# Performance work log

Hardware: AMD Instinct MI355X
Metric: run time of the kernel (lower is better)

The kernel has to match this reference:

```python
import jax, jax.numpy as jnp
import numpy as np

D_MODEL = 512
N_HEADS = 8
HIDDEN = 2048  # mlp_ratio * d_model
B, N = 2, 1024

# 2^dim sign-flip frames for FrameAveraging(dim=2)
_FRAME_OPS = jnp.array([[1., 1.], [1., -1.], [-1., 1.], [-1., -1.]], jnp.float32)


def _ln(x, g, b, eps=1e-5):
    mu = jnp.mean(x, axis=-1, keepdims=True)
    var = jnp.mean((x - mu) ** 2, axis=-1, keepdims=True)
    return (x - mu) * jax.lax.rsqrt(var + eps) * g + b


def setup_inputs() -> dict:
    key = jax.random.key(0)
    ks = jax.random.split(key, 8)
    s = 0.02
    return {
        "token_embs": jax.random.normal(ks[0], (B, N, D_MODEL), jnp.float32),
        "coords": jax.random.normal(ks[1], (B, N, 2), jnp.float32),
        "padding_mask": jnp.zeros((B, N, N), jnp.bool_),
        "ln1_g": jnp.ones((D_MODEL,), jnp.float32),
        "ln1_b": jnp.zeros((D_MODEL,), jnp.float32),
        "w_qkv": jax.random.normal(ks[2], (D_MODEL, 3 * D_MODEL), jnp.float32) * s,
        "b_qkv": jnp.zeros((3 * D_MODEL,), jnp.float32),
        "w_edge": jax.random.normal(ks[3], (3, N_HEADS), jnp.float32) * s,
        "w_out": jax.random.normal(ks[4], (D_MODEL, D_MODEL), jnp.float32) * s,
        "b_out": jnp.zeros((D_MODEL,), jnp.float32),
        "ln2_g": jnp.ones((D_MODEL,), jnp.float32),
        "ln2_b": jnp.zeros((D_MODEL,), jnp.float32),
        "w1": jax.random.normal(ks[5], (D_MODEL, HIDDEN), jnp.float32) * s,
        "b1": jnp.zeros((HIDDEN,), jnp.float32),
        "w2": jax.random.normal(ks[6], (HIDDEN, D_MODEL), jnp.float32) * s,
        "b2": jnp.zeros((D_MODEL,), jnp.float32),
    }


def _block(x, coords, pad_mask, ln1_g, ln1_b, w_qkv, b_qkv, w_edge, w_out, b_out,
           ln2_g, ln2_b, w1, b1, w2, b2):
    Bb, Nn, C = x.shape
    H = w_edge.shape[1]
    d = C // H
    scale = d ** -0.5
    nf = _FRAME_OPS.shape[0]

    # ---- attention QKV ----
    qkv = _ln(x, ln1_g, ln1_b) @ w_qkv + b_qkv
    q, k, v = jnp.split(qkv, 3, axis=-1)
    q = q.reshape(Bb, Nn, H, d).transpose(0, 2, 1, 3) * scale  # (B,H,N,d)
    k = k.reshape(Bb, Nn, H, d).transpose(0, 2, 1, 3)
    v = v.reshape(Bb, Nn, H, d).transpose(0, 2, 1, 3)
    attn = jnp.einsum('bhnd,bhmd->bhnm', q, k)

    # ---- pairwise radial coords + frame averaging ----
    rc = coords[:, :, None, :] - coords[:, None, :, :]           # (B,N,N,2)
    rnorm = jnp.linalg.norm(rc, axis=-1).reshape(Bb * Nn, Nn, 1)
    rc = rc.reshape(Bb * Nn, Nn, 2)                              # (M,N,2)
    valid = (~pad_mask).reshape(Bb * Nn, Nn)
    m = valid.astype(rc.dtype)[..., None]                        # (M,N,1)
    center = jnp.sum(rc * m, axis=1) / jnp.sum(m, axis=1)        # masked mean
    Xc = (rc - center[:, None]) * m                              # (M,N,2)
    Cov = jnp.einsum('mni,mnj->mij', Xc, Xc)                     # (M,2,2)
    _, V = jnp.linalg.eigh(jax.lax.stop_gradient(Cov))           # PCA frame (detached)
    F_ops = _FRAME_OPS[None, :, None, :] * V[:, None]            # (M,nf,2,2) sign-flipped eigvecs
    h = jnp.einsum('moji,mpj->mopi', F_ops, Xc) * m[:, None]     # (M,nf,N,2)

    feat = jnp.concatenate(
        [h, jnp.broadcast_to(rnorm[:, None], (Bb * Nn, nf, Nn, 1))], axis=-1)  # (M,nf,N,3)
    bias = jnp.einsum('monk,kh->monh', feat, w_edge).mean(axis=1)  # (M,N,H)
    bias = bias.reshape(Bb, Nn, Nn, H).transpose(0, 3, 1, 2)       # (B,H,N,N)

    attn = attn + bias
    attn = jnp.where(pad_mask[:, None], jnp.float32(-1e9), attn)
    attn = jax.nn.softmax(attn, axis=-1)
    o = jnp.einsum('bhnm,bhmd->bhnd', attn, v)
    o = o.transpose(0, 2, 1, 3).reshape(Bb, Nn, C) @ w_out + b_out

    x = x + o
    y = _ln(x, ln2_g, ln2_b)
    y = jax.nn.gelu(y @ w1 + b1, approximate=False) @ w2 + b2
    return x + y


def reference(token_embs, coords, padding_mask, ln1_g, ln1_b, w_qkv, b_qkv, w_edge,
              w_out, b_out, ln2_g, ln2_b, w1, b1, w2, b2):
    return _block(token_embs, coords, padding_mask, ln1_g, ln1_b, w_qkv, b_qkv,
                  w_edge, w_out, b_out, ln2_g, ln2_b, w1, b1, w2, b2)
```

## Files before the change

kernel.cpp:

```cpp
#include <hip/hip_runtime.h>
#include <hip/hip_bf16.h>
#include <math.h>

#define NHEADS 8
#define NTOK   1024
#define MTOK   2048

typedef __attribute__((ext_vector_type(8))) short  sh8;
typedef __attribute__((ext_vector_type(8))) __bf16 bf16x8;
typedef __attribute__((ext_vector_type(4))) float  f32x4;
typedef __attribute__((ext_vector_type(4))) unsigned int u32x4;

__device__ __forceinline__ short f2bf(float v) {
    return __builtin_bit_cast(short, __float2bfloat16(v));
}
__device__ __forceinline__ float bf2f(short v) {
    return __builtin_bit_cast(float, ((unsigned)(unsigned short)v) << 16);
}
__device__ __forceinline__ float ex2(float v) {
    return __builtin_amdgcn_exp2f(v);
}
__device__ __forceinline__ f32x4 mfma16(sh8 a, sh8 b, f32x4 c) {
    return __builtin_amdgcn_mfma_f32_16x16x32_bf16(
        __builtin_bit_cast(bf16x8, a), __builtin_bit_cast(bf16x8, b), c, 0, 0, 0);
}
__device__ __forceinline__ void aload16(void* lds, const void* g) {
    __builtin_amdgcn_global_load_lds(
        (const __attribute__((address_space(1))) unsigned int*)g,
        (__attribute__((address_space(3))) unsigned int*)lds, 16, 0, 0);
}

#define LOG2E 1.4426950408889634f

template<bool FUSE>
__global__ __launch_bounds__(256) void ln_bf16(const float* __restrict__ x,
    const float* __restrict__ g, const float* __restrict__ bta, short* __restrict__ y,
    const float* __restrict__ bias2, float* __restrict__ resout)
{
    int row = blockIdx.x, t = threadIdx.x;
    const float* xr = x + (size_t)row * 512;
    float2 v = *reinterpret_cast<const float2*>(&xr[t*2]);
    float s = v.x + v.y, ss = v.x*v.x + v.y*v.y;
    #pragma unroll
    for (int m = 1; m < 64; m <<= 1) { s += __shfl_xor(s, m); ss += __shfl_xor(ss, m); }
    __shared__ float red[8];
    int wid = t >> 6, lane = t & 63;
    if (!lane) { red[wid] = s; red[4+wid] = ss; }
    __syncthreads();
    s = red[0]+red[1]+red[2]+red[3]; ss = red[4]+red[5]+red[6]+red[7];
    float mu = s*(1.f/512), var = ss*(1.f/512) - mu*mu, rs = rsqrtf(var + 1e-5f);
    float2 gg = *reinterpret_cast<const float2*>(&g[t*2]);
    float2 bb = *reinterpret_cast<const float2*>(&bta[t*2]);
    short2 o; o.x = f2bf((v.x-mu)*rs*gg.x + bb.x); o.y = f2bf((v.y-mu)*rs*gg.y + bb.y);
    *reinterpret_cast<short2*>(&y[(size_t)row*512 + t*2]) = o;
    if (FUSE) {
        float2 b2 = *reinterpret_cast<const float2*>(&bias2[t*2]);
        float2 ro = {v.x + b2.x, v.y + b2.y};
        *reinterpret_cast<float2*>(&resout[(size_t)row*512 + t*2]) = ro;
    }
}

__global__ __launch_bounds__(256) void wconv2x(
    const float* __restrict__ W0, short* __restrict__ WT0, int K0, int N0, int nb0,
    const float* __restrict__ W1, short* __restrict__ WT1, int K1, int N1)
{
    const float* W; short* WT; int K, N, bid;
    if ((int)blockIdx.x < nb0) { W = W0; WT = WT0; K = K0; N = N0; bid = blockIdx.x; }
    else                       { W = W1; WT = WT1; K = K1; N = N1; bid = blockIdx.x - nb0; }
    int nbx = N >> 5;
    int bn = (bid % nbx) * 32, bk = (bid / nbx) * 32;
    __shared__ float t[32][33];
    int c = threadIdx.x & 31, r8 = threadIdx.x >> 5;
    #pragma unroll
    for (int i = 0; i < 4; ++i) {
        int r = r8 + i*8;
        t[r][c] = W[(size_t)(bk + r)*N + bn + c];
    }
    __syncthreads();
    #pragma unroll
    for (int i = 0; i < 4; ++i) {
        int r = r8 + i*8;
        WT[(size_t)(bn + r)*K + bk + c] = f2bf(t[c][r]);
    }
}

__global__ __launch_bounds__(256) void prep(const float* __restrict__ coords,
    const unsigned char* __restrict__ mask, short* __restrict__ rnP,
    unsigned long long* __restrict__ mbP)
{
    __shared__ float2 kc_s[64];
    __shared__ float2 qc_s[16];
    int bid = blockIdx.x;
    int bqt = bid >> 4, jt = bid & 15;
    int b = bqt >> 6, qt = bqt & 63;
    int t = threadIdx.x, w = t >> 6, lane = t & 63;
    int lr = lane & 15, lg = lane >> 4;

    if (t < 64)            kc_s[t]      = *reinterpret_cast<const float2*>(&coords[(size_t)(b*1024 + jt*64 + t)*2]);
    else if (t < 80)       qc_s[t - 64] = *reinterpret_cast<const float2*>(&coords[(size_t)(b*1024 + qt*16 + (t - 64))*2]);
    __syncthreads();

    float2 qc = qc_s[lr];
    short4 o;
    short* op = &o.x;
    #pragma unroll
    for (int r = 0; r < 4; ++r) {
        float2 kc = kc_s[w*16 + lg*4 + r];
        float dx = qc.x - kc.x, dy = qc.y - kc.y;
        op[r] = f2bf(sqrtf(dx*dx + dy*dy));
    }
    *reinterpret_cast<short4*>(&rnP[(size_t)((bid*4 + w)*256) + lane*4]) = o;

    #pragma unroll
    for (int i = 0; i < 4; ++i) {
        int q = w*4 + i;
        unsigned char v = mask[(size_t)(b*1024 + qt*16 + q)*NTOK + jt*64 + lane];
        unsigned long long bits = __ballot(v != 0);
        if (!lane) mbP[(size_t)bid*16 + q] = bits;
    }
}

template<int EPI, bool OUTBF, bool BIAS_ROW, int SPLITK, bool QSC, int NT>
__global__ __launch_bounds__(256) void gemm64(
    const short* __restrict__ A, const short* __restrict__ BT,
    const float* __restrict__ bias, const float* __restrict__ res,
    void* __restrict__ Cout, int M, int N, int K, int nbx)
{
    __shared__ sh8 As8[3][512];
    __shared__ sh8 Bs8[3][512];
    int tid = threadIdx.x;
    int w = tid >> 6, lane = tid & 63, lr = lane & 15, lg = lane >> 4;
    int wr = w >> 1, wc = w & 1;
    int cpx = gridDim.x >> 3;
    int swz = (blockIdx.x & 7)*cpx + (blockIdx.x >> 3);
    int bx = swz % nbx, by = swz / nbx;
    int bm0 = by*64, bn0 = bx*64;
    int kbeg = (K / SPLITK) * blockIdx.z;

    f32x4 zero = {0.f,0.f,0.f,0.f};
    f32x4 acc[2][2];
    #pragma unroll
    for (int m = 0; m < 2; ++m)
        #pragma unroll
        for (int n = 0; n < 2; ++n) acc[m][n] = zero;

    #define STAGE(buf, k0) { \
        _Pragma("unroll") \
        for (int it = 0; it < 2; ++it) { \
            int s = tid + it*256; \
            int r = s >> 3, g = s & 7; \
            int ksw = (k0) + ((g ^ (r & 7)) << 3); \
            aload16(&As8[buf][s], A  + (size_t)(bm0 + r)*K + ksw); \
            aload16(&Bs8[buf][s], BT + (size_t)(bn0 + r)*K + ksw); \
        } }

    STAGE(0, kbeg)
    if (NT > 1) STAGE(1, kbeg + 64)

    #pragma unroll
    for (int t = 0; t < NT; ++t) {
        if (t + 1 < NT) asm volatile("s_waitcnt vmcnt(4)" ::: "memory");
        else            asm volatile("s_waitcnt vmcnt(0)" ::: "memory");
        __builtin_amdgcn_s_barrier();
        __builtin_amdgcn_sched_barrier(0);
        int buf = t % 3;
        sh8 af[2][2], bfv[2][2];
        #pragma unroll
        for (int m = 0; m < 2; ++m) {
            int R = wr*32 + m*16 + lr;
            #pragma unroll
            for (int s = 0; s < 2; ++s) af[m][s] = As8[buf][R*8 + ((s*4+lg) ^ (R & 7))];
        }
        #pragma unroll
        for (int n = 0; n < 2; ++n) {
            int R = wc*32 + n*16 + lr;
            #pragma unroll
            for (int s = 0; s < 2; ++s) bfv[n][s] = Bs8[buf][R*8 + ((s*4+lg) ^ (R & 7))];
        }
        if (t + 2 < NT) STAGE((t+2)%3, kbeg + (t+2)*64)
        #pragma unroll
        for (int m = 0; m < 2; ++m)
            #pragma unroll
            for (int n = 0; n < 2; ++n)
                #pragma unroll
                for (int s = 0; s < 2; ++s)
                    acc[m][n] = mfma16(af[m][s], bfv[n][s], acc[m][n]);
        asm volatile("s_waitcnt lgkmcnt(0)" ::: "memory");
    }
    #undef STAGE

    #pragma unroll
    for (int m = 0; m < 2; ++m) {
        #pragma unroll
        for (int n = 0; n < 2; ++n) {
            #pragma unroll
            for (int r = 0; r < 4; ++r) {
                int row = bm0 + wr*32 + m*16 + lg*4 + r;
                int col = bn0 + wc*32 + n*16 + lr;
                if (EPI == 3) {
                    atomicAdd((float*)Cout + (size_t)row*N + col, acc[m][n][r]);
                } else {
                    float v = acc[m][n][r] + (BIAS_ROW ? bias[row] : bias[col]);
                    if (QSC && col < 512) v *= (0.125f * LOG2E);
                    if (EPI == 1) v += res[(size_t)row*N + col];
                    if (EPI == 2) v = 0.5f * v * (1.0f + erff(v * 0.70710678f));
                    if (OUTBF) ((short*)Cout)[(size_t)row*N + col] = f2bf(v);
                    else       ((float*)Cout)[(size_t)row*N + col] = v;
                }
            }
        }
    }
}

__global__ __launch_bounds__(256) void attn_reg(
    const short* __restrict__ qk, const short* __restrict__ vt,
    const short* __restrict__ rnP, const unsigned long long* __restrict__ mbP,
    const float* __restrict__ w_edge, short* __restrict__ OpA,
    short* __restrict__ OpB, float* __restrict__ ml)
{
    __shared__ sh8 Ks8[2][512];
    __shared__ sh8 Vs8[2][512];

    int cpx = gridDim.x >> 3;
    int swz = (blockIdx.x & 7)*cpx + (blockIdx.x >> 3);
    int w = threadIdx.x >> 6, lane = threadIdx.x & 63;
    int lr = lane & 15, lg = lane >> 4;
    int qb = swz & 15;
    int h  = (swz >> 4) & 7;
    int b  = (swz >> 7) & 1;
    int ks = swz >> 8;

    const int q0 = qb*64 + w*16;
    const int qrow0 = b*NTOK + q0;
    const int jt0 = ks*4;
    const int bqt = b*64 + qb*4 + w;

    sh8 qf[2];
    #pragma unroll
    for (int s = 0; s < 2; ++s)
        qf[s] = *reinterpret_cast<const sh8*>(qk + (size_t)(qrow0 + lr)*1024 + h*64 + s*32 + lg*8);

    float we2l = w_edge[2*NHEADS + h] * LOG2E;

    float m_i = -1e30f, l_lane = 0.f;
    f32x4 zero = {0.f,0.f,0.f,0.f};
    f32x4 accO[4];
    #pragma unroll
    for (int n = 0; n < 4; ++n) accO[n] = zero;

    const short* kbase = qk + 512 + h*64;
    const short* vbase = vt + (size_t)h*64*2048 + b*NTOK;
    int sr = threadIdx.x >> 3, sg = threadIdx.x & 7;
    int sx = (sg ^ (sr & 7)) << 3;

    #define ASTAGE(bf, jt) { \
        aload16(&Ks8[bf][threadIdx.x],       kbase + (size_t)(b*NTOK + (jt)*64 + sr)*1024 + sx); \
        aload16(&Ks8[bf][threadIdx.x + 256], kbase + (size_t)(b*NTOK + (jt)*64 + sr + 32)*1024 + sx); \
        aload16(&Vs8[bf][threadIdx.x],       vbase + (size_t)sr*2048 + (jt)*64 + sx); \
        aload16(&Vs8[bf][threadIdx.x + 256], vbase + (size_t)(sr + 32)*2048 + (jt)*64 + sx); \
    }

    short4 rn_reg[2][4];
    unsigned long long mr_reg[2];
    #define RMLOAD(bf, jt) { \
        _Pragma("unroll") \
        for (int n = 0; n < 4; ++n) \
            rn_reg[bf][n] = *reinterpret_cast<const short4*>( \
                &rnP[(size_t)(((bqt*16 + (jt))*4 + n)*256) + lane*4]); \
        mr_reg[bf] = mbP[(size_t)(bqt*16 + (jt))*16 + lr]; \
    }

    ASTAGE(0, jt0)
    RMLOAD(0, jt0)

    #pragma unroll
    for (int t = 0; t < 4; ++t) {
        if (t == 0) asm volatile("s_waitcnt vmcnt(0)" ::: "memory");
        else        asm volatile("s_waitcnt vmcnt(5)" ::: "memory");
        __builtin_amdgcn_s_barrier();
        __builtin_amdgcn_sched_barrier(0);
        int buf = t & 1;

        if (t + 1 < 4) {
            ASTAGE(buf ^ 1, jt0 + t + 1)
            RMLOAD(buf ^ 1, jt0 + t + 1)
        }

        f32x4 Sv[4];
        #pragma unroll
        for (int n = 0; n < 4; ++n) {
            int kcol = n*16 + lr;
            sh8 k0v = Ks8[buf][kcol*8 + (lg       ^ (kcol & 7))];
            sh8 k1v = Ks8[buf][kcol*8 + ((4 + lg) ^ (kcol & 7))];
            Sv[n] = mfma16(k1v, qf[1], mfma16(k0v, qf[0], zero));
        }

        #pragma unroll
        for (int n = 0; n < 4; ++n) {
            short4 rn4 = rn_reg[buf][n];
            Sv[n][0] = fmaf(bf2f(rn4.x), we2l, Sv[n][0]);
            Sv[n][1] = fmaf(bf2f(rn4.y), we2l, Sv[n][1]);
            Sv[n][2] = fmaf(bf2f(rn4.z), we2l, Sv[n][2]);
            Sv[n][3] = fmaf(bf2f(rn4.w), we2l, Sv[n][3]);
        }

        float mx = Sv[0][0];
        #pragma unroll
        for (int n = 0; n < 4; ++n)
            #pragma unroll
            for (int r = 0; r < 4; ++r) mx = fmaxf(mx, Sv[n][r]);
        mx = fmaxf(mx, __shfl_xor(mx, 16));
        mx = fmaxf(mx, __shfl_xor(mx, 32));
        float mnew = fmaxf(m_i, mx);
        float f = ex2(m_i - mnew);
        m_i = mnew;

        unsigned long long mr = mr_reg[buf];
        float ps = 0.f;
        unsigned pk[8];
        #pragma unroll
        for (int n = 0; n < 4; ++n) {
            float p_[4];
            #pragma unroll
            for (int r = 0; r < 4; ++r) {
                float p = ex2(Sv[n][r] - mnew);
                p = ((mr >> (n*16 + lg*4 + r)) & 1ull) ? 0.f : p;
                ps += p;
                p_[r] = p;
            }
            pk[2*n]   = ((unsigned)(unsigned short)f2bf(p_[1]) << 16) | (unsigned short)f2bf(p_[0]);
            pk[2*n+1] = ((unsigned)(unsigned short)f2bf(p_[3]) << 16) | (unsigned short)f2bf(p_[2]);
        }
        l_lane = l_lane * f + ps;

        int src0 = lr + ((lg & 1) << 5);
        int src1 = src0 + 16;
        sh8 pa[2];
        #pragma unroll
        for (int s = 0; s < 2; ++s) {
            int ns = 2*s + (lg >> 1);
            u32x4 dv;
            dv.x = (unsigned)__shfl((int)pk[2*ns],   src0);
            dv.y = (unsigned)__shfl((int)pk[2*ns+1], src0);
            dv.z = (unsigned)__shfl((int)pk[2*ns],   src1);
            dv.w = (unsigned)__shfl((int)pk[2*ns+1], src1);
            pa[s] = __builtin_bit_cast(sh8, dv);
        }

        float fb[4];
        #pragma unroll
        for (int r = 0; r < 4; ++r) fb[r] = __shfl(f, lg*4 + r);
        #pragma unroll
        for (int n = 0; n < 4; ++n)
            #pragma unroll
            for (int r = 0; r < 4; ++r) accO[n][r] *= fb[r];

        #pragma unroll
        for (int n = 0; n < 4; ++n) {
            int dcol = n*16 + lr;
            sh8 v0 = Vs8[buf][dcol*8 + (lg       ^ (dcol & 7))];
            sh8 v1 = Vs8[buf][dcol*8 + ((4 + lg) ^ (dcol & 7))];
            accO[n] = mfma16(pa[1], v1, mfma16(pa[0], v0, accO[n]));
        }

        asm volatile("s_waitcnt lgkmcnt(0)" ::: "memory");
    }
    #undef ASTAGE
    #undef RMLOAD

    l_lane += __shfl_xor(l_lane, 16);
    l_lane += __shfl_xor(l_lane, 32);

    short* Op = (ks < 2) ? OpA : OpB;
    #pragma unroll
    for (int r = 0; r < 4; ++r) {
        size_t row = (size_t)((ks & 1)*MTOK + qrow0 + lg*4 + r);
        #pragma unroll
        for (int n = 0; n < 4; ++n)
            Op[row*512 + h*64 + n*16 + lr] = f2bf(accO[n][r]);
    }
    if (lg == 0) {
        size_t mrow = (size_t)(ks*MTOK + qrow0 + lr);
        ml[(mrow*NHEADS + h)*2 + 0] = m_i;
        ml[(mrow*NHEADS + h)*2 + 1] = l_lane;
    }
}

__global__ __launch_bounds__(256) void attn_combine4(const short* __restrict__ OpA,
    const short* __restrict__ OpB, const float* __restrict__ ml,
    short* __restrict__ ob)
{
    int idx = blockIdx.x*256 + threadIdx.x;
    int tok = idx >> 7, dd = (idx & 127) * 4;
    int h = dd >> 6;
    float m[4], l[4];
    #pragma unroll
    for (int s = 0; s < 4; ++s) {
        m[s] = ml[(((size_t)s*MTOK + tok)*NHEADS + h)*2 + 0];
        l[s] = ml[(((size_t)s*MTOK + tok)*NHEADS + h)*2 + 1];
    }
    float mm = fmaxf(fmaxf(m[0], m[1]), fmaxf(m[2], m[3]));
    float wsum = 0.f, a0 = 0.f, a1 = 0.f, a2 = 0.f, a3 = 0.f;
    #pragma unroll
    for (int s = 0; s < 4; ++s) {
        float wv = ex2(m[s] - mm);
        wsum += wv * l[s];
        const short* Op = (s < 2) ? OpA : OpB;
        short4 p = *reinterpret_cast<const short4*>(&Op[((size_t)((s&1)*MTOK) + tok)*512 + dd]);
        a0 += bf2f(p.x)*wv; a1 += bf2f(p.y)*wv;
        a2 += bf2f(p.z)*wv; a3 += bf2f(p.w)*wv;
    }
    float inv = 1.f / wsum;
    short4 o;
    o.x = f2bf(a0*inv); o.y = f2bf(a1*inv);
    o.z = f2bf(a2*inv); o.w = f2bf(a3*inv);
    *reinterpret_cast<short4*>(&ob[(size_t)tok*512 + dd]) = o;
}

extern "C" void kernel_launch(void* const* d_in, const int* in_sizes, int n_in,
                              void* d_out, int out_size, void* d_ws, size_t ws_size,
                              hipStream_t stream)
{
    const float* x      = (const float*)d_in[0];
    const float* coords = (const float*)d_in[1];
    const unsigned char* mask = (const unsigned char*)d_in[2];
    const float* ln1_g = (const float*)d_in[3];
    const float* ln1_b = (const float*)d_in[4];
    const float* w_qkv = (const float*)d_in[5];
    const float* b_qkv = (const float*)d_in[6];
    const float* w_edge= (const float*)d_in[7];
    const float* w_out = (const float*)d_in[8];
    const float* b_out = (const float*)d_in[9];
    const float* ln2_g = (const float*)d_in[10];
    const float* ln2_b = (const float*)d_in[11];
    const float* w1    = (const float*)d_in[12];
    const float* b1    = (const float*)d_in[13];
    const float* w2    = (const float*)d_in[14];
    const float* b2    = (const float*)d_in[15];
    float* out = (float*)d_out;

    char* W = (char*)d_ws;
    const size_t MB = 1024*1024;
    float* x1    = (float*)(W);
    short* qk    = (short*)(W + 4*MB);
    short* vtb   = (short*)(W + 8*MB);
    short* woutT = (short*)(W + 10*MB);
    short* xln   = (short*)(W + 10*MB + 512*1024);
    short* wqkvT = (short*)(W + 12*MB + 512*1024);
    short* OpB   = (short*)(W + 10*MB + 512*1024);
    short* OpA   = (short*)(W + 14*MB + 512*1024);
    short* rnP   = (short*)(W + 18*MB + 512*1024);
    float* mlp   = (float*)(W + 22*MB + 512*1024);
    unsigned long long* mbP = (unsigned long long*)(W + 23*MB);
    short* ob    = (short*)(W + 6*MB);
    short* y     = xln;
    short* w1T   = (short*)(W + 4*MB);
    short* w2T   = (short*)(W + 8*MB);
    short* hid   = (short*)(W + 14*MB + 512*1024);

    prep<<<dim3(2048,1,1), 256, 0, stream>>>(coords, mask, rnP, mbP);
    wconv2x<<<dim3(1024,1,1), 256, 0, stream>>>(w_qkv, wqkvT, 512, 1536, 768,
                                                w_out, woutT, 512, 512);
    ln_bf16<false><<<MTOK, 256, 0, stream>>>(x, ln1_g, ln1_b, xln, nullptr, nullptr);
    gemm64<0,true,false,1,true,8><<<dim3(512,1,1), 256, 0, stream>>>(
        xln, wqkvT, b_qkv, nullptr, qk, MTOK, 1024, 512, 16);
    gemm64<0,true,true,1,false,8><<<dim3(256,1,1), 256, 0, stream>>>(
        wqkvT + (size_t)1024*512, xln, b_qkv + 1024, nullptr, vtb, 512, MTOK, 512, 32);
    attn_reg<<<dim3(1024,1,1), 256, 0, stream>>>(qk, vtb, rnP, mbP, w_edge, OpA, OpB, mlp);
    attn_combine4<<<dim3(1024,1,1), 256, 0, stream>>>(OpA, OpB, mlp, ob);
    gemm64<1,false,false,1,false,8><<<dim3(256,1,1), 256, 0, stream>>>(
        ob, woutT, b_out, x, x1, MTOK, 512, 512, 8);
    wconv2x<<<dim3(2048,1,1), 256, 0, stream>>>(w1, w1T, 512, 2048, 1024,
                                                w2, w2T, 2048, 512);
    ln_bf16<true><<<MTOK, 256, 0, stream>>>(x1, ln2_g, ln2_b, y, b2, out);
    gemm64<2,true,false,1,false,8><<<dim3(1024,1,1), 256, 0, stream>>>(
        y, w1T, b1, nullptr, hid, MTOK, 2048, 512, 32);
    gemm64<3,false,false,2,false,16><<<dim3(256,1,2), 256, 0, stream>>>(
        hid, w2T, nullptr, nullptr, out, MTOK, 512, 2048, 8);
}
```

Baseline: 92.84 us.

## Add 64x32 GEMM tiles, drop split-K atomics, lazy softmax rescale, packed bf16 cvt

Adds a gemm32n kernel with 64x32 output tiles and uses it for the V projection, the output projection and the second MLP GEMM. This doubles the block count on the narrow GEMMs and replaces the split-K atomicAdd path, whose residual and bias were pre-written by the fused LN, with a plain epilogue that adds bias and residual. In attention, the online-softmax rescale is skipped unless some row max grows by more than 8 (log2 domain), and probabilities are packed to bf16 with v_cvt_pk_bf16_f32. The lazy rescale lets p values reach up to 2^8, which risks bf16 precision loss, and the unsplit second MLP GEMM now runs a 32-step K loop per block.

Result: no change. 92.32 us (-0.6%).

```diff
diff --git a/kernel.cpp b/kernel.cpp
--- a/kernel.cpp
+++ b/kernel.cpp
@@ -32,10 +32,8 @@
 
 #define LOG2E 1.4426950408889634f
 
-template<bool FUSE>
 __global__ __launch_bounds__(256) void ln_bf16(const float* __restrict__ x,
-    const float* __restrict__ g, const float* __restrict__ bta, short* __restrict__ y,
-    const float* __restrict__ bias2, float* __restrict__ resout)
+    const float* __restrict__ g, const float* __restrict__ bta, short* __restrict__ y)
 {
     int row = blockIdx.x, t = threadIdx.x;
     const float* xr = x + (size_t)row * 512;
@@ -53,11 +51,6 @@
     float2 bb = *reinterpret_cast<const float2*>(&bta[t*2]);
     short2 o; o.x = f2bf((v.x-mu)*rs*gg.x + bb.x); o.y = f2bf((v.y-mu)*rs*gg.y + bb.y);
     *reinterpret_cast<short2*>(&y[(size_t)row*512 + t*2]) = o;
-    if (FUSE) {
-        float2 b2 = *reinterpret_cast<const float2*>(&bias2[t*2]);
-        float2 ro = {v.x + b2.x, v.y + b2.y};
-        *reinterpret_cast<float2*>(&resout[(size_t)row*512 + t*2]) = ro;
-    }
 }
 
 __global__ __launch_bounds__(256) void wconv2x(
@@ -120,7 +113,7 @@
     }
 }
 
-template<int EPI, bool OUTBF, bool BIAS_ROW, int SPLITK, bool QSC, int NT>
+template<int EPI, bool OUTBF, bool BIAS_ROW, bool QSC, int NT>
 __global__ __launch_bounds__(256) void gemm64(
     const short* __restrict__ A, const short* __restrict__ BT,
     const float* __restrict__ bias, const float* __restrict__ res,
@@ -135,7 +128,6 @@
     int swz = (blockIdx.x & 7)*cpx + (blockIdx.x >> 3);
     int bx = swz % nbx, by = swz / nbx;
     int bm0 = by*64, bn0 = bx*64;
-    int kbeg = (K / SPLITK) * blockIdx.z;
 
     f32x4 zero = {0.f,0.f,0.f,0.f};
     f32x4 acc[2][2];
@@ -154,8 +146,8 @@
             aload16(&Bs8[buf][s], BT + (size_t)(bn0 + r)*K + ksw); \
         } }
 
-    STAGE(0, kbeg)
-    if (NT > 1) STAGE(1, kbeg + 64)
+    STAGE(0, 0)
+    if (NT > 1) STAGE(1, 64)
 
     #pragma unroll
     for (int t = 0; t < NT; ++t) {
@@ -177,7 +169,7 @@
             #pragma unroll
             for (int s = 0; s < 2; ++s) bfv[n][s] = Bs8[buf][R*8 + ((s*4+lg) ^ (R & 7))];
         }
-        if (t + 2 < NT) STAGE((t+2)%3, kbeg + (t+2)*64)
+        if (t + 2 < NT) STAGE((t+2)%3, (t+2)*64)
         #pragma unroll
         for (int m = 0; m < 2; ++m)
             #pragma unroll
@@ -197,17 +189,89 @@
             for (int r = 0; r < 4; ++r) {
                 int row = bm0 + wr*32 + m*16 + lg*4 + r;
                 int col = bn0 + wc*32 + n*16 + lr;
-                if (EPI == 3) {
-                    atomicAdd((float*)Cout + (size_t)row*N + col, acc[m][n][r]);
-                } else {
-                    float v = acc[m][n][r] + (BIAS_ROW ? bias[row] : bias[col]);
-                    if (QSC && col < 512) v *= (0.125f * LOG2E);
-                    if (EPI == 1) v += res[(size_t)row*N + col];
-                    if (EPI == 2) v = 0.5f * v * (1.0f + erff(v * 0.70710678f));
-                    if (OUTBF) ((short*)Cout)[(size_t)row*N + col] = f2bf(v);
-                    else       ((float*)Cout)[(size_t)row*N + col] = v;
-                }
+                float v = acc[m][n][r] + (BIAS_ROW ? bias[row] : bias[col]);
+                if (QSC && col < 512) v *= (0.125f * LOG2E);
+                if (EPI == 1) v += res[(size_t)row*N + col];
+                if (EPI == 2) v = 0.5f * v * (1.0f + erff(v * 0.70710678f));
+                if (OUTBF) ((short*)Cout)[(size_t)row*N + col] = f2bf(v);
+                else       ((float*)Cout)[(size_t)row*N + col] = v;
             }
+        }
+    }
+}
+
+template<int EPI, bool OUTBF, bool BIAS_ROW, int NT>
+__global__ __launch_bounds__(256) void gemm32n(
+    const short* __restrict__ A, const short* __restrict__ BT,
+    const float* __restrict__ bias, const float* __restrict__ res,
+    void* __restrict__ Cout, int M, int N, int K, int nbx)
+{
+    __shared__ sh8 As8[3][512];
+    __shared__ sh8 Bs8[3][256];
+    int tid = threadIdx.x;
+    int w = tid >> 6, lane = tid & 63, lr = lane & 15, lg = lane >> 4;
+    int cpx = gridDim.x >> 3;
+    int swz = (blockIdx.x & 7)*cpx + (blockIdx.x >> 3);
+    int bx = swz % nbx, by = swz / nbx;
+    int bm0 = by*64, bn0 = bx*32;
+
+    f32x4 zero = {0.f,0.f,0.f,0.f};
+    f32x4 acc[2];
+    acc[0] = zero; acc[1] = zero;
+
+    #define STAGE32(buf, k0) { \
+        _Pragma("unroll") \
+        for (int it = 0; it < 2; ++it) { \
+            int s = tid + it*256; \
+            int r = s >> 3, g = s & 7; \
+            int ksw = (k0) + ((g ^ (r & 7)) << 3); \
+            aload16(&As8[buf][s], A + (size_t)(bm0 + r)*K + ksw); \
+        } \
+        { int r = tid >> 3, g = tid & 7; \
+          int ksw = (k0) + ((g ^ (r & 7)) << 3); \
+          aload16(&Bs8[buf][tid], BT + (size_t)(bn0 + r)*K + ksw); } }
+
+    STAGE32(0, 0)
+    if (NT > 1) STAGE32(1, 64)
+
+    #pragma unroll
+    for (int t = 0; t < NT; ++t) {
+        if (t + 1 < NT) asm volatile("s_waitcnt vmcnt(3)" ::: "memory");
+        else            asm volatile("s_waitcnt vmcnt(0)" ::: "memory");
+        __builtin_amdgcn_s_barrier();
+        __builtin_amdgcn_sched_barrier(0);
+        int buf = t % 3;
+        sh8 af[2], bfv[2][2];
+        int Ra = w*16 + lr;
+        #pragma unroll
+        for (int s = 0; s < 2; ++s) af[s] = As8[buf][Ra*8 + ((s*4+lg) ^ (Ra & 7))];
+        #pragma unroll
+        for (int n = 0; n < 2; ++n) {
+            int R = n*16 + lr;
+            #pragma unroll
+            for (int s = 0; s < 2; ++s) bfv[n][s] = Bs8[buf][R*8 + ((s*4+lg) ^ (R & 7))];
+        }
+        if (t + 2 < NT) STAGE32((t+2)%3, (t+2)*64)
+        #pragma unroll
+        for (int n = 0; n < 2; ++n)
+            #pragma unroll
+            for (int s = 0; s < 2; ++s)
+                acc[n] = mfma16(af[s], bfv[n][s], acc[n]);
+        asm volatile("s_waitcnt lgkmcnt(0)" ::: "memory");
+    }
+    #undef STAGE32
+
+    #pragma unroll
+    for (int n = 0; n < 2; ++n) {
+        #pragma unroll
+        for (int r = 0; r < 4; ++r) {
+            int row = bm0 + w*16 + lg*4 + r;
+            int col = bn0 + n*16 + lr;
+            float v = acc[n][r] + (BIAS_ROW ? bias[row] : bias[col]);
+            if (EPI == 1) v += res[(size_t)row*N + col];
+            if (EPI == 2) v = 0.5f * v * (1.0f + erff(v * 0.70710678f));
+            if (OUTBF) ((short*)Cout)[(size_t)row*N + col] = f2bf(v);
+            else       ((float*)Cout)[(size_t)row*N + col] = v;
         }
     }
 }
@@ -311,9 +375,20 @@
             for (int r = 0; r < 4; ++r) mx = fmaxf(mx, Sv[n][r]);
         mx = fmaxf(mx, __shfl_xor(mx, 16));
         mx = fmaxf(mx, __shfl_xor(mx, 32));
-        float mnew = fmaxf(m_i, mx);
-        float f = ex2(m_i - mnew);
-        m_i = mnew;
+
+        if (!__all(mx <= m_i + 8.0f)) {
+            float mnew = fmaxf(m_i, mx);
+            float f = ex2(m_i - mnew);
+            m_i = mnew;
+            l_lane *= f;
+            float fb[4];
+            #pragma unroll
+            for (int r = 0; r < 4; ++r) fb[r] = __shfl(f, lg*4 + r);
+            #pragma unroll
+            for (int n = 0; n < 4; ++n)
+                #pragma unroll
+                for (int r = 0; r < 4; ++r) accO[n][r] *= fb[r];
+        }
 
         unsigned long long mr = mr_reg[buf];
         float ps = 0.f;
@@ -323,15 +398,15 @@
             float p_[4];
             #pragma unroll
             for (int r = 0; r < 4; ++r) {
-                float p = ex2(Sv[n][r] - mnew);
+                float p = ex2(Sv[n][r] - m_i);
                 p = ((mr >> (n*16 + lg*4 + r)) & 1ull) ? 0.f : p;
                 ps += p;
                 p_[r] = p;
             }
-            pk[2*n]   = ((unsigned)(unsigned short)f2bf(p_[1]) << 16) | (unsigned short)f2bf(p_[0]);
-            pk[2*n+1] = ((unsigned)(unsigned short)f2bf(p_[3]) << 16) | (unsigned short)f2bf(p_[2]);
-        }
-        l_lane = l_lane * f + ps;
+            asm("v_cvt_pk_bf16_f32 %0, %1, %2" : "=v"(pk[2*n])   : "v"(p_[0]), "v"(p_[1]));
+            asm("v_cvt_pk_bf16_f32 %0, %1, %2" : "=v"(pk[2*n+1]) : "v"(p_[2]), "v"(p_[3]));
+        }
+        l_lane += ps;
 
         int src0 = lr + ((lg & 1) << 5);
         int src1 = src0 + 16;
@@ -346,14 +421,6 @@
             dv.w = (unsigned)__shfl((int)pk[2*ns+1], src1);
             pa[s] = __builtin_bit_cast(sh8, dv);
         }
-
-        float fb[4];
-        #pragma unroll
-        for (int r = 0; r < 4; ++r) fb[r] = __shfl(f, lg*4 + r);
-        #pragma unroll
-        for (int n = 0; n < 4; ++n)
-            #pragma unroll
-            for (int r = 0; r < 4; ++r) accO[n][r] *= fb[r];
 
         #pragma unroll
         for (int n = 0; n < 4; ++n) {
@@ -461,20 +528,20 @@
     prep<<<dim3(2048,1,1), 256, 0, stream>>>(coords, mask, rnP, mbP);
     wconv2x<<<dim3(1024,1,1), 256, 0, stream>>>(w_qkv, wqkvT, 512, 1536, 768,
                                                 w_out, woutT, 512, 512);
-    ln_bf16<false><<<MTOK, 256, 0, stream>>>(x, ln1_g, ln1_b, xln, nullptr, nullptr);
-    gemm64<0,true,false,1,true,8><<<dim3(512,1,1), 256, 0, stream>>>(
+    ln_bf16<<<MTOK, 256, 0, stream>>>(x, ln1_g, ln1_b, xln);
+    gemm64<0,true,false,true,8><<<dim3(512,1,1), 256, 0, stream>>>(
         xln, wqkvT, b_qkv, nullptr, qk, MTOK, 1024, 512, 16);
-    gemm64<0,true,true,1,false,8><<<dim3(256,1,1), 256, 0, stream>>>(
-        wqkvT + (size_t)1024*512, xln, b_qkv + 1024, nullptr, vtb, 512, MTOK, 512, 32);
+    gemm32n<0,true,true,8><<<dim3(512,1,1), 256, 0, stream>>>(
+        wqkvT + (size_t)1024*512, xln, b_qkv + 1024, nullptr, vtb, 512, MTOK, 512, 64);
     attn_reg<<<dim3(1024,1,1), 256, 0, stream>>>(qk, vtb, rnP, mbP, w_edge, OpA, OpB, mlp);
     attn_combine4<<<dim3(1024,1,1), 256, 0, stream>>>(OpA, OpB, mlp, ob);
-    gemm64<1,false,false,1,false,8><<<dim3(256,1,1), 256, 0, stream>>>(
-        ob, woutT, b_out, x, x1, MTOK, 512, 512, 8);
+    gemm32n<1,false,false,8><<<dim3(512,1,1), 256, 0, stream>>>(
+        ob, woutT, b_out, x, x1, MTOK, 512, 512, 16);
     wconv2x<<<dim3(2048,1,1), 256, 0, stream>>>(w1, w1T, 512, 2048, 1024,
                                                 w2, w2T, 2048, 512);
-    ln_bf16<true><<<MTOK, 256, 0, stream>>>(x1, ln2_g, ln2_b, y, b2, out);
-    gemm64<2,true,false,1,false,8><<<dim3(1024,1,1), 256, 0, stream>>>(
+    ln_bf16<<<MTOK, 256, 0, stream>>>(x1, ln2_g, ln2_b, y);
+    gemm64<2,true,false,false,8><<<dim3(1024,1,1), 256, 0, stream>>>(
         y, w1T, b1, nullptr, hid, MTOK, 2048, 512, 32);
-    gemm64<3,false,false,2,false,16><<<dim3(256,1,2), 256, 0, stream>>>(
-        hid, w2T, nullptr, nullptr, out, MTOK, 512, 2048, 8);
-}
+    gemm32n<1,false,false,32><<<dim3(512,1,1), 256, 0, stream>>>(
+        hid, w2T, b2, x1, out, MTOK, 512, 2048, 16);
+}
```
